# Optimization experiments

Hardware: AMD Instinct MI355X
Metric: run time of the kernel (lower is better)

Reference implementation:

```python
import jax, jax.numpy as jnp
import numpy as np

B, C, H, W, T = 16, 1024, 32, 32, 77
NUM_HEADS = 8


def setup_inputs() -> dict:
    key = jax.random.key(0)
    ks = jax.random.split(key, 8)
    s = 0.02
    return {
        "Vx": jax.random.normal(ks[0], (B, C, H, W), dtype=jnp.float32),
        "Tx": jax.random.normal(ks[1], (B, C, T), dtype=jnp.float32),
        "Wq": jax.random.normal(ks[2], (C, C), dtype=jnp.float32) * s,
        "bq": jax.random.normal(ks[3], (C,), dtype=jnp.float32) * s,
        "Wkv": jax.random.normal(ks[4], (2 * C, C), dtype=jnp.float32) * s,
        "bkv": jax.random.normal(ks[5], (2 * C,), dtype=jnp.float32) * s,
        "Wp": jax.random.normal(ks[6], (C, C), dtype=jnp.float32) * s,
        "bp": jax.random.normal(ks[7], (C,), dtype=jnp.float32) * s,
    }


def reference(Vx, Tx, Wq, bq, Wkv, bkv, Wp, bp):
    b, c, h, w = Vx.shape
    n = h * w
    nh = NUM_HEADS
    hd = c // nh
    scale = float(hd) ** (-0.5)  # scale = (dim/num_heads)**-0.5

    # 1x1 conv2d q projection: (B,C,H,W) -> (B,nh,hd,N)
    q = jnp.einsum("bchw,dc->bdhw", Vx, Wq) + bq[None, :, None, None]
    q = q.reshape(b, nh, hd, n)

    # 1x1 conv1d kv projection: (B,C,T) -> (B,nh,2*hd,T), then per-head split
    kv = jnp.einsum("bct,dc->bdt", Tx, Wkv) + bkv[None, :, None]
    kv = kv.reshape(b, nh, 2 * hd, -1)
    k, v = kv[:, :, :hd, :], kv[:, :, hd:, :]

    # attn: (B,nh,N,T) = q^T k, softmax over T
    attn = jax.nn.softmax(jnp.einsum("bhdn,bhdt->bhnt", q, k) * scale, axis=-1)

    # out: v @ attn^T -> (B,nh,hd,N) -> (B,C,H,W)
    out = jnp.einsum("bhdt,bhnt->bhdn", v, attn).reshape(b, c, h, w)

    # 1x1 conv2d output projection
    return jnp.einsum("bchw,dc->bdhw", out, Wp) + bp[None, :, None, None]
```

## Files before the change

kernel.cpp:

```cpp
#include <hip/hip_runtime.h>
#include <cstdint>
#include <cstddef>

typedef unsigned short u16;
typedef __bf16 bf16x8 __attribute__((ext_vector_type(8)));
typedef float f32x4 __attribute__((ext_vector_type(4)));

typedef __attribute__((address_space(1))) const void global_cvoid;
typedef __attribute__((address_space(3))) void lds_void;

__device__ __forceinline__ void async16(void* lds, const void* g) {
  __builtin_amdgcn_global_load_lds((global_cvoid*)g, (lds_void*)lds, 16, 0, 0);
}

__device__ __forceinline__ u16 f2bf(float f) {
  uint32_t u = __float_as_uint(f);
  return (u16)((u + 0x7fffu + ((u >> 16) & 1u)) >> 16);
}

__device__ __forceinline__ void pack4_hlh(uint32_t* dst, const float* v) {
  u16 h[4], l[4];
#pragma unroll
  for (int u = 0; u < 4; ++u) {
    h[u] = f2bf(v[u]);
    float hf = __uint_as_float((uint32_t)h[u] << 16);
    l[u] = f2bf(v[u] - hf);
  }
  dst[0] = (uint32_t)h[0] | ((uint32_t)l[0] << 16);
  dst[1] = (uint32_t)h[0] | ((uint32_t)h[1] << 16);
  dst[2] = (uint32_t)l[1] | ((uint32_t)h[1] << 16);
  dst[3] = (uint32_t)h[2] | ((uint32_t)l[2] << 16);
  dst[4] = (uint32_t)h[2] | ((uint32_t)h[3] << 16);
  dst[5] = (uint32_t)l[3] | ((uint32_t)h[3] << 16);
}

__device__ __forceinline__ void pack4_hhl(uint32_t* dst, const float* v) {
  u16 h[4], l[4];
#pragma unroll
  for (int u = 0; u < 4; ++u) {
    h[u] = f2bf(v[u]);
    float hf = __uint_as_float((uint32_t)h[u] << 16);
    l[u] = f2bf(v[u] - hf);
  }
  dst[0] = (uint32_t)h[0] | ((uint32_t)h[0] << 16);
  dst[1] = (uint32_t)l[0] | ((uint32_t)h[1] << 16);
  dst[2] = (uint32_t)h[1] | ((uint32_t)l[1] << 16);
  dst[3] = (uint32_t)h[2] | ((uint32_t)h[2] << 16);
  dst[4] = (uint32_t)l[2] | ((uint32_t)h[3] << 16);
  dst[5] = (uint32_t)h[3] | ((uint32_t)l[3] << 16);
}

__global__ __launch_bounds__(256) void pack_w(const float* __restrict__ W,
                                              u16* __restrict__ out) {
  int idx = blockIdx.x * 256 + threadIdx.x;
  int d = idx >> 10, c = idx & 1023;
  float f = W[idx];
  u16 h = f2bf(f);
  float hf = __uint_as_float((uint32_t)h << 16);
  u16 l = f2bf(f - hf);
  u16* dst = out + (size_t)d * 3072 + 3 * c;
  dst[0] = h; dst[1] = h; dst[2] = l;
}

__global__ __launch_bounds__(256) void pack_x(const float* __restrict__ X,
                                              u16* __restrict__ out) {
  const int b = blockIdx.z, c0 = blockIdx.y * 32, n0 = blockIdx.x * 32;
  __shared__ float tile[32][33];
  const float* src = X + ((size_t)b * 1024 + c0) * 1024 + n0;
  const int tc = threadIdx.x >> 5, tn = threadIdx.x & 31;
#pragma unroll
  for (int i = 0; i < 4; ++i)
    tile[tc + i * 8][tn] = src[(size_t)(tc + i * 8) * 1024 + tn];
  __syncthreads();
  const int nl = threadIdx.x >> 3, cg = (threadIdx.x & 7) * 4;
  float v[4];
#pragma unroll
  for (int u = 0; u < 4; ++u) v[u] = tile[cg + u][nl];
  uint32_t* dst = (uint32_t*)(out + ((size_t)b * 1024 + n0 + nl) * 3072 +
                              (size_t)(c0 + cg) * 3);
  pack4_hlh(dst, v);
}

__global__ __launch_bounds__(256) void pack_tx(const float* __restrict__ Tx,
                                               u16* __restrict__ out) {
  const int b = blockIdx.z, c0 = blockIdx.y * 32, t0 = blockIdx.x * 32;
  __shared__ float tile[32][33];
  const float* src = Tx + ((size_t)b * 1024 + c0) * 77;
  const int tc = threadIdx.x >> 5, tn = threadIdx.x & 31;
#pragma unroll
  for (int i = 0; i < 4; ++i) {
    int t = t0 + tn;
    tile[tc + i * 8][tn] = (t < 77) ? src[(size_t)(tc + i * 8) * 77 + t] : 0.f;
  }
  __syncthreads();
  const int nl = threadIdx.x >> 3, cg = (threadIdx.x & 7) * 4;
  float v[4];
#pragma unroll
  for (int u = 0; u < 4; ++u) v[u] = tile[cg + u][nl];
  uint32_t* dst = (uint32_t*)(out + ((size_t)b * 128 + t0 + nl) * 3072 +
                              (size_t)(c0 + cg) * 3);
  pack4_hlh(dst, v);
}

__global__ __launch_bounds__(256) void pack_kt(const float* __restrict__ kv,
                                               u16* __restrict__ out) {
  const int h = blockIdx.x, b = blockIdx.y;
  __shared__ float sk[128][81];
  const float* src = kv + ((size_t)b * 2048 + h * 256) * 80;
#pragma unroll
  for (int it = 0; it < 40; ++it) {
    int idx = it * 256 + threadIdx.x;
    sk[idx / 80][idx % 80] = src[idx];
  }
  __syncthreads();
#pragma unroll
  for (int it = 0; it < 10; ++it) {
    int idx = it * 256 + threadIdx.x;
    int t = idx >> 5, dg = (idx & 31) * 4;
    float v[4];
#pragma unroll
    for (int u = 0; u < 4; ++u) v[u] = sk[dg + u][t];
    uint32_t* dst = (uint32_t*)(out + ((size_t)(b * 8 + h) * 80 + t) * 384 +
                                (size_t)3 * dg);
    pack4_hhl(dst, v);
  }
}

__global__ __launch_bounds__(256) void pack_v(const float* __restrict__ kv,
                                              u16* __restrict__ out) {
  const int h = blockIdx.x, b = blockIdx.y;
  const float* src = kv + ((size_t)b * 2048 + h * 256 + 128) * 80;
  u16* ob = out + (size_t)(b * 8 + h) * 128 * 256;
#pragma unroll
  for (int it = 0; it < 10; ++it) {
    int idx = it * 256 + threadIdx.x;
    int d = idx / 20, tg = idx % 20;
    float4 v4 = *(const float4*)(src + (size_t)d * 80 + tg * 4);
    float v[4] = {v4.x, v4.y, v4.z, v4.w};
    uint32_t* dst = (uint32_t*)(ob + (size_t)d * 256 + 12 * tg);
    pack4_hlh(dst, v);
  }
  {
    int row = threadIdx.x >> 1, part = threadIdx.x & 1;
    *(uint4*)(ob + (size_t)row * 256 + 240 + part * 8) = make_uint4(0, 0, 0, 0);
  }
}

template <int OUTMODE>
__global__ __launch_bounds__(512, 2) void gemm_mfma(
    const u16* __restrict__ Apk, const u16* __restrict__ Bpk,
    const float* __restrict__ bias, void* __restrict__ Yv)
{
  const int b  = blockIdx.z;
  const int d0 = blockIdx.y * 256;
  const int n0 = blockIdx.x * 256;
  const int tid  = threadIdx.x;
  const int lane = tid & 63;
  const int w    = tid >> 6;
  const int wm   = w >> 2, wn = w & 3;
  const int lr   = lane & 15;
  const int lkb  = (lane >> 4) * 16;

  __shared__ __align__(16) char smem[131072];

  const u16* Bb = Bpk + (size_t)b * 1024 * 3072;

  const char* gsrc[4];
  int ldst[4];
#pragma unroll
  for (int f = 0; f < 4; ++f) {
    int g = w * 4 + f;
    if (g < 16) {
      gsrc[f] = (const char*)(Apk + (size_t)(d0 + g * 16 + lr) * 3072) + lkb;
      ldst[f] = g * 1024;
    } else {
      gsrc[f] = (const char*)(Bb + (size_t)(n0 + (g - 16) * 16 + lr) * 3072) + lkb;
      ldst[f] = 16384 + (g - 16) * 1024;
    }
  }

  auto stage = [&](int t) {
    char* base = smem + (t & 3) * 32768;
#pragma unroll
    for (int f = 0; f < 4; ++f)
      async16(base + ldst[f], gsrc[f] + (size_t)t * 64);
  };

  f32x4 acc[8][4];
#pragma unroll
  for (int i = 0; i < 8; ++i)
#pragma unroll
    for (int j = 0; j < 4; ++j) acc[i][j] = (f32x4){0.f, 0.f, 0.f, 0.f};

  stage(0); stage(1); stage(2); stage(3);
  asm volatile("s_waitcnt vmcnt(12)" ::: "memory");
  __builtin_amdgcn_s_barrier();

  for (int t = 0; t < 96; ++t) {
    const char* bufA = smem + (size_t)(t & 3) * 32768 + (size_t)lane * 16;
    const char* bufB = bufA + 16384;

    bf16x8 af[4], bfv[4];
#pragma unroll
    for (int i = 0; i < 4; ++i)
      af[i] = *(const bf16x8*)(bufA + (wm * 8 + i) * 1024);
#pragma unroll
    for (int j = 0; j < 4; ++j)
      bfv[j] = *(const bf16x8*)(bufB + (wn * 4 + j) * 1024);
    asm volatile("" ::: "memory");
    __builtin_amdgcn_s_barrier();
    asm volatile("s_waitcnt lgkmcnt(0)" ::: "memory");
    __builtin_amdgcn_sched_barrier(0);
    __builtin_amdgcn_s_setprio(1);
#pragma unroll
    for (int i = 0; i < 4; ++i)
#pragma unroll
      for (int j = 0; j < 4; ++j)
        acc[i][j] = __builtin_amdgcn_mfma_f32_16x16x32_bf16(af[i], bfv[j], acc[i][j], 0, 0, 0);
    __builtin_amdgcn_s_setprio(0);

#pragma unroll
    for (int i = 0; i < 4; ++i)
      af[i] = *(const bf16x8*)(bufA + (wm * 8 + 4 + i) * 1024);
    asm volatile("s_waitcnt lgkmcnt(0)" ::: "memory");
    __builtin_amdgcn_sched_barrier(0);
    if (t < 93)       asm volatile("s_waitcnt vmcnt(8)" ::: "memory");
    else if (t == 93) asm volatile("s_waitcnt vmcnt(4)" ::: "memory");
    else if (t == 94) asm volatile("s_waitcnt vmcnt(0)" ::: "memory");
    __builtin_amdgcn_s_barrier();
    if (t + 4 < 96) stage(t + 4);
    __builtin_amdgcn_s_setprio(1);
#pragma unroll
    for (int i = 0; i < 4; ++i)
#pragma unroll
      for (int j = 0; j < 4; ++j)
        acc[4 + i][j] = __builtin_amdgcn_mfma_f32_16x16x32_bf16(af[i], bfv[j], acc[4 + i][j], 0, 0, 0);
    __builtin_amdgcn_s_setprio(0);
  }

#pragma unroll
  for (int i = 0; i < 8; ++i) {
    const int dbase = d0 + wm * 128 + i * 16 + (lane >> 4) * 4;
    const float4 bv = *(const float4*)(bias + dbase);
#pragma unroll
    for (int j = 0; j < 4; ++j) {
      const int n = n0 + wn * 64 + j * 16 + lr;
      if (OUTMODE == 0) {
        float* yp = (float*)Yv + ((size_t)b * 1024 + dbase) * 1024 + n;
        yp[0]        = acc[i][j].x + bv.x;
        yp[1024]     = acc[i][j].y + bv.y;
        yp[2 * 1024] = acc[i][j].z + bv.z;
        yp[3 * 1024] = acc[i][j].w + bv.w;
      } else {
        float v[4] = {acc[i][j].x + bv.x, acc[i][j].y + bv.y,
                      acc[i][j].z + bv.z, acc[i][j].w + bv.w};
        uint32_t* dst = (uint32_t*)((u16*)Yv +
                                    ((size_t)b * 1024 + n) * 3072 + 3 * dbase);
        pack4_hlh(dst, v);
      }
    }
  }
}

__global__ __launch_bounds__(256) void gemm_kv_mfma(
    const u16* __restrict__ Apk, const u16* __restrict__ Bpk,
    const float* __restrict__ bias, float* __restrict__ Y)
{
  const int b  = blockIdx.y;
  const int d0 = blockIdx.x * 128;
  const int tid  = threadIdx.x;
  const int lane = tid & 63;
  const int w    = tid >> 6;
  const int wm   = w >> 1, wn = w & 1;

  __shared__ __align__(16) char smem[65536];

  const int lr = lane & 15;
  const int lk = (lane >> 4) * 8;

  const u16* Bb = Bpk + (size_t)b * 128 * 3072;
  const char* gA0 = (const char*)(Apk + ((size_t)(d0 + (w * 2 + 0) * 16 + lr) * 3072 + lk));
  const char* gA1 = (const char*)(Apk + ((size_t)(d0 + (w * 2 + 1) * 16 + lr) * 3072 + lk));
  const char* gB0 = (const char*)(Bb  + ((size_t)((w * 2 + 0) * 16 + lr) * 3072 + lk));
  const char* gB1 = (const char*)(Bb  + ((size_t)((w * 2 + 1) * 16 + lr) * 3072 + lk));

  auto stage = [&](int p, int ks) {
    char* ba = smem + p * 32768 + (w * 2) * 1024;
    char* bb = ba + 16384;
    const int kb = ks * 128;
#pragma unroll
    for (int k2 = 0; k2 < 2; ++k2) {
      async16(ba + k2 * 8192,        gA0 + kb + k2 * 64);
      async16(ba + k2 * 8192 + 1024, gA1 + kb + k2 * 64);
      async16(bb + k2 * 8192,        gB0 + kb + k2 * 64);
      async16(bb + k2 * 8192 + 1024, gB1 + kb + k2 * 64);
    }
  };

  f32x4 acc[4][4];
#pragma unroll
  for (int i = 0; i < 4; ++i)
#pragma unroll
    for (int j = 0; j < 4; ++j) acc[i][j] = (f32x4){0.f, 0.f, 0.f, 0.f};

  stage(0, 0);
  stage(1, 1);

  for (int ks = 0; ks < 48; ++ks) {
    if (ks < 47) asm volatile("s_waitcnt vmcnt(8)" ::: "memory");
    else         asm volatile("s_waitcnt vmcnt(0)" ::: "memory");
    __builtin_amdgcn_s_barrier();

    const int p = ks & 1;
    const char* baseA = smem + p * 32768 + wm * 4096 + lane * 16;
    const char* baseB = smem + p * 32768 + 16384 + wn * 4096 + lane * 16;
#pragma unroll
    for (int k2 = 0; k2 < 2; ++k2) {
      bf16x8 af[4], bfv[4];
#pragma unroll
      for (int i = 0; i < 4; ++i) {
        af[i]  = *(const bf16x8*)(baseA + k2 * 8192 + i * 1024);
        bfv[i] = *(const bf16x8*)(baseB + k2 * 8192 + i * 1024);
      }
#pragma unroll
      for (int i = 0; i < 4; ++i)
#pragma unroll
        for (int j = 0; j < 4; ++j)
          acc[i][j] = __builtin_amdgcn_mfma_f32_16x16x32_bf16(af[i], bfv[j], acc[i][j], 0, 0, 0);
    }

    asm volatile("" ::: "memory");
    __builtin_amdgcn_s_barrier();
    if (ks + 2 < 48) stage(p, ks + 2);
  }

#pragma unroll
  for (int i = 0; i < 4; ++i) {
    const int dbase = d0 + wm * 64 + i * 16 + (lane >> 4) * 4;
    const float4 bv = *(const float4*)(bias + dbase);
#pragma unroll
    for (int j = 0; j < 4; ++j) {
      const int n = wn * 64 + j * 16 + lr;
      if (n < 80) {
        float* yp = Y + ((size_t)b * 2048 + dbase) * 80 + n;
        yp[0]      = acc[i][j].x + bv.x;
        yp[80]     = acc[i][j].y + bv.y;
        yp[160]    = acc[i][j].z + bv.z;
        yp[240]    = acc[i][j].w + bv.w;
      }
    }
  }
}

__global__ __launch_bounds__(256, 2) void attn_mfma(
    const u16* __restrict__ qpk,
    const u16* __restrict__ ktpk,
    const u16* __restrict__ vpk,
    u16* __restrict__ xout)
{
  const int b  = blockIdx.z;
  const int h  = blockIdx.y;
  const int n0 = blockIdx.x * 128;
  const int tid  = threadIdx.x;
  const int w    = tid >> 6;
  const int lane = tid & 63;
  const int lr = lane & 15;
  const int lc = lane >> 4;
  const float scale = 0.08838834764831845f;

  __shared__ u16 Plds[4][32 * 256];
  u16* Pw = &Plds[w][0];

  {
    int row = lane & 31, part = lane >> 5;
    *(uint4*)&Pw[row * 256 + 240 + part * 8] = make_uint4(0, 0, 0, 0);
  }

  const u16* qb = qpk + ((size_t)b * 1024 + n0 + w * 32 + lr) * 3072 +
                  384 * h + lc * 8;
  const u16* kb = ktpk + (size_t)(b * 8 + h) * 80 * 384 + (size_t)lr * 384 + lc * 8;

  f32x4 accs[2][5];
#pragma unroll
  for (int ni = 0; ni < 2; ++ni)
#pragma unroll
    for (int tt = 0; tt < 5; ++tt) accs[ni][tt] = (f32x4){0.f, 0.f, 0.f, 0.f};

  for (int ks = 0; ks < 12; ++ks) {
    bf16x8 qa[2], kt[5];
    qa[0] = *(const bf16x8*)(qb + ks * 32);
    qa[1] = *(const bf16x8*)(qb + 16 * 3072 + ks * 32);
#pragma unroll
    for (int tt = 0; tt < 5; ++tt)
      kt[tt] = *(const bf16x8*)(kb + (size_t)tt * 16 * 384 + ks * 32);
#pragma unroll
    for (int ni = 0; ni < 2; ++ni)
#pragma unroll
      for (int tt = 0; tt < 5; ++tt)
        accs[ni][tt] = __builtin_amdgcn_mfma_f32_16x16x32_bf16(qa[ni], kt[tt], accs[ni][tt], 0, 0, 0);
  }

  if (lr >= 13) {
    accs[0][4] = (f32x4){-3.0e38f, -3.0e38f, -3.0e38f, -3.0e38f};
    accs[1][4] = (f32x4){-3.0e38f, -3.0e38f, -3.0e38f, -3.0e38f};
  }

#pragma unroll
  for (int ni = 0; ni < 2; ++ni) {
    f32x4 mx = accs[ni][0];
#pragma unroll
    for (int tt = 1; tt < 5; ++tt) {
      mx.x = fmaxf(mx.x, accs[ni][tt].x);
      mx.y = fmaxf(mx.y, accs[ni][tt].y);
      mx.z = fmaxf(mx.z, accs[ni][tt].z);
      mx.w = fmaxf(mx.w, accs[ni][tt].w);
    }
#pragma unroll
    for (int mk = 1; mk <= 8; mk <<= 1) {
      mx.x = fmaxf(mx.x, __shfl_xor(mx.x, mk));
      mx.y = fmaxf(mx.y, __shfl_xor(mx.y, mk));
      mx.z = fmaxf(mx.z, __shfl_xor(mx.z, mk));
      mx.w = fmaxf(mx.w, __shfl_xor(mx.w, mk));
    }
    f32x4 sm = (f32x4){0.f, 0.f, 0.f, 0.f};
#pragma unroll
    for (int tt = 0; tt < 5; ++tt) {
      f32x4 e;
      e.x = __expf((accs[ni][tt].x - mx.x) * scale);
      e.y = __expf((accs[ni][tt].y - mx.y) * scale);
      e.z = __expf((accs[ni][tt].z - mx.z) * scale);
      e.w = __expf((accs[ni][tt].w - mx.w) * scale);
      accs[ni][tt] = e;
      sm += e;
    }
#pragma unroll
    for (int mk = 1; mk <= 8; mk <<= 1) {
      sm.x += __shfl_xor(sm.x, mk);
      sm.y += __shfl_xor(sm.y, mk);
      sm.z += __shfl_xor(sm.z, mk);
      sm.w += __shfl_xor(sm.w, mk);
    }
    f32x4 inv = (f32x4){1.f / sm.x, 1.f / sm.y, 1.f / sm.z, 1.f / sm.w};
#pragma unroll
    for (int tt = 0; tt < 5; ++tt) {
#pragma unroll
      for (int c = 0; c < 4; ++c) {
        float pv = accs[ni][tt][c] * inv[c];
        int row = ni * 16 + lc * 4 + c;
        int t = tt * 16 + lr;
        u16 hh = f2bf(pv);
        float hf = __uint_as_float((uint32_t)hh << 16);
        u16 ll = f2bf(pv - hf);
        u16* pp = &Pw[row * 256 + 3 * t];
        pp[0] = hh; pp[1] = hh; pp[2] = ll;
      }
    }
  }

  f32x4 acco[2][8];
#pragma unroll
  for (int ni = 0; ni < 2; ++ni)
#pragma unroll
    for (int dj = 0; dj < 8; ++dj) acco[ni][dj] = (f32x4){0.f, 0.f, 0.f, 0.f};

  const u16* vb = vpk + (size_t)(b * 8 + h) * 128 * 256 + (size_t)lr * 256 + lc * 8;
  const u16* pb = &Pw[lr * 256 + lc * 8];

  for (int ks = 0; ks < 8; ++ks) {
    bf16x8 pa[2], vv[8];
    pa[0] = *(const bf16x8*)(pb + ks * 32);
    pa[1] = *(const bf16x8*)(pb + 16 * 256 + ks * 32);
#pragma unroll
    for (int dj = 0; dj < 8; ++dj)
      vv[dj] = *(const bf16x8*)(vb + (size_t)dj * 16 * 256 + ks * 32);
#pragma unroll
    for (int ni = 0; ni < 2; ++ni)
#pragma unroll
      for (int dj = 0; dj < 8; ++dj)
        acco[ni][dj] = __builtin_amdgcn_mfma_f32_16x16x32_bf16(pa[ni], vv[dj], acco[ni][dj], 0, 0, 0);
  }

  float* Pf = (float*)Pw;
#pragma unroll
  for (int ni = 0; ni < 2; ++ni)
#pragma unroll
    for (int dj = 0; dj < 8; ++dj) {
      const int dl = dj * 16 + lr;
#pragma unroll
      for (int c = 0; c < 4; ++c)
        Pf[(ni * 16 + lc * 4 + c) * 128 + dl] = acco[ni][dj][c];
    }

  const int prow = lane >> 5;
  const int pgrp = lane & 31;
#pragma unroll
  for (int r2 = 0; r2 < 16; ++r2) {
    const int row = r2 * 2 + prow;
    f32x4 vv4 = *(const f32x4*)&Pf[row * 128 + pgrp * 4];
    float v[4] = {vv4.x, vv4.y, vv4.z, vv4.w};
    uint32_t* dst = (uint32_t*)(xout +
        ((size_t)b * 1024 + n0 + w * 32 + row) * 3072 + 384 * h + 12 * pgrp);
    pack4_hlh(dst, v);
  }
}

extern "C" void kernel_launch(void* const* d_in, const int* in_sizes, int n_in,
                              void* d_out, int out_size, void* d_ws, size_t ws_size,
                              hipStream_t stream) {
  const float* Vx  = (const float*)d_in[0];
  const float* Tx  = (const float*)d_in[1];
  const float* Wq  = (const float*)d_in[2];
  const float* bq  = (const float*)d_in[3];
  const float* Wkv = (const float*)d_in[4];
  const float* bkv = (const float*)d_in[5];
  const float* Wp  = (const float*)d_in[6];
  const float* bp  = (const float*)d_in[7];
  float* out = (float*)d_out;

  char* ws = (char*)d_ws;
  const size_t MiB = (size_t)1 << 20;
  u16*   Xpk      = (u16*)(ws + 0);
  u16*   qpk      = (u16*)(ws + 96 * MiB);
  u16*   WqPk     = (u16*)(ws + 192 * MiB);
  u16*   KTpk     = (u16*)(ws + 192 * MiB);
  u16*   WkvPk    = (u16*)(ws + 198 * MiB);
  u16*   Vpk      = (u16*)(ws + 200 * MiB);
  u16*   TxPk     = (u16*)(ws + 210 * MiB);
  float* kvbuf    = (float*)(ws + 222 * MiB);
  u16*   WpPk     = (u16*)(ws + 233 * MiB);

  pack_w<<<4096, 256, 0, stream>>>(Wq, WqPk);
  pack_w<<<4096, 256, 0, stream>>>(Wp, WpPk);
  pack_w<<<8192, 256, 0, stream>>>(Wkv, WkvPk);
  pack_x<<<dim3(32, 32, 16), 256, 0, stream>>>(Vx, Xpk);
  pack_tx<<<dim3(4, 32, 16), 256, 0, stream>>>(Tx, TxPk);
  gemm_mfma<1><<<dim3(4, 4, 16), 512, 0, stream>>>(WqPk, Xpk, bq, qpk);
  gemm_kv_mfma<<<dim3(16, 16), 256, 0, stream>>>(WkvPk, TxPk, bkv, kvbuf);
  pack_kt<<<dim3(8, 16), 256, 0, stream>>>(kvbuf, KTpk);
  pack_v<<<dim3(8, 16), 256, 0, stream>>>(kvbuf, Vpk);
  attn_mfma<<<dim3(8, 8, 16), 256, 0, stream>>>(qpk, KTpk, Vpk, Xpk);
  gemm_mfma<0><<<dim3(4, 4, 16), 512, 0, stream>>>(WpPk, Xpk, bp, out);
}
```

Measured before the change: 544.0 us.

## Deepen kv GEMM pipeline to four stages and drop mid-iteration barrier in main GEMM

```diff
diff --git a/kernel.cpp b/kernel.cpp
--- a/kernel.cpp
+++ b/kernel.cpp
@@ -200,17 +200,13 @@
     const char* bufA = smem + (size_t)(t & 3) * 32768 + (size_t)lane * 16;
     const char* bufB = bufA + 16384;
 
-    bf16x8 af[4], bfv[4];
+    bf16x8 af[4], bfv[4], af2[4];
 #pragma unroll
     for (int i = 0; i < 4; ++i)
       af[i] = *(const bf16x8*)(bufA + (wm * 8 + i) * 1024);
 #pragma unroll
     for (int j = 0; j < 4; ++j)
       bfv[j] = *(const bf16x8*)(bufB + (wn * 4 + j) * 1024);
-    asm volatile("" ::: "memory");
-    __builtin_amdgcn_s_barrier();
-    asm volatile("s_waitcnt lgkmcnt(0)" ::: "memory");
-    __builtin_amdgcn_sched_barrier(0);
     __builtin_amdgcn_s_setprio(1);
 #pragma unroll
     for (int i = 0; i < 4; ++i)
@@ -221,20 +217,21 @@
 
 #pragma unroll
     for (int i = 0; i < 4; ++i)
-      af[i] = *(const bf16x8*)(bufA + (wm * 8 + 4 + i) * 1024);
+      af2[i] = *(const bf16x8*)(bufA + (wm * 8 + 4 + i) * 1024);
     asm volatile("s_waitcnt lgkmcnt(0)" ::: "memory");
     __builtin_amdgcn_sched_barrier(0);
     if (t < 93)       asm volatile("s_waitcnt vmcnt(8)" ::: "memory");
     else if (t == 93) asm volatile("s_waitcnt vmcnt(4)" ::: "memory");
-    else if (t == 94) asm volatile("s_waitcnt vmcnt(0)" ::: "memory");
+    else              asm volatile("s_waitcnt vmcnt(0)" ::: "memory");
     __builtin_amdgcn_s_barrier();
+    asm volatile("" ::: "memory");
     if (t + 4 < 96) stage(t + 4);
     __builtin_amdgcn_s_setprio(1);
 #pragma unroll
     for (int i = 0; i < 4; ++i)
 #pragma unroll
       for (int j = 0; j < 4; ++j)
-        acc[4 + i][j] = __builtin_amdgcn_mfma_f32_16x16x32_bf16(af[i], bfv[j], acc[4 + i][j], 0, 0, 0);
+        acc[4 + i][j] = __builtin_amdgcn_mfma_f32_16x16x32_bf16(af2[i], bfv[j], acc[4 + i][j], 0, 0, 0);
     __builtin_amdgcn_s_setprio(0);
   }
 
@@ -272,29 +269,30 @@
   const int lane = tid & 63;
   const int w    = tid >> 6;
   const int wm   = w >> 1, wn = w & 1;
+  const int lr   = lane & 15;
+  const int lkb  = (lane >> 4) * 16;
 
   __shared__ __align__(16) char smem[65536];
 
-  const int lr = lane & 15;
-  const int lk = (lane >> 4) * 8;
-
   const u16* Bb = Bpk + (size_t)b * 128 * 3072;
-  const char* gA0 = (const char*)(Apk + ((size_t)(d0 + (w * 2 + 0) * 16 + lr) * 3072 + lk));
-  const char* gA1 = (const char*)(Apk + ((size_t)(d0 + (w * 2 + 1) * 16 + lr) * 3072 + lk));
-  const char* gB0 = (const char*)(Bb  + ((size_t)((w * 2 + 0) * 16 + lr) * 3072 + lk));
-  const char* gB1 = (const char*)(Bb  + ((size_t)((w * 2 + 1) * 16 + lr) * 3072 + lk));
-
-  auto stage = [&](int p, int ks) {
-    char* ba = smem + p * 32768 + (w * 2) * 1024;
-    char* bb = ba + 16384;
-    const int kb = ks * 128;
-#pragma unroll
-    for (int k2 = 0; k2 < 2; ++k2) {
-      async16(ba + k2 * 8192,        gA0 + kb + k2 * 64);
-      async16(ba + k2 * 8192 + 1024, gA1 + kb + k2 * 64);
-      async16(bb + k2 * 8192,        gB0 + kb + k2 * 64);
-      async16(bb + k2 * 8192 + 1024, gB1 + kb + k2 * 64);
-    }
+
+  const char* gsrc[4];
+  int ldst[4];
+#pragma unroll
+  for (int f = 0; f < 4; ++f) {
+    int g = w * 4 + f;
+    if (g < 8)
+      gsrc[f] = (const char*)(Apk + (size_t)(d0 + g * 16 + lr) * 3072) + lkb;
+    else
+      gsrc[f] = (const char*)(Bb + (size_t)((g - 8) * 16 + lr) * 3072) + lkb;
+    ldst[f] = g * 1024;
+  }
+
+  auto stage = [&](int t) {
+    char* base = smem + (t & 3) * 16384;
+#pragma unroll
+    for (int f = 0; f < 4; ++f)
+      async16(base + ldst[f], gsrc[f] + (size_t)t * 64);
   };
 
   f32x4 acc[4][4];
@@ -303,35 +301,45 @@
 #pragma unroll
     for (int j = 0; j < 4; ++j) acc[i][j] = (f32x4){0.f, 0.f, 0.f, 0.f};
 
-  stage(0, 0);
-  stage(1, 1);
-
-  for (int ks = 0; ks < 48; ++ks) {
-    if (ks < 47) asm volatile("s_waitcnt vmcnt(8)" ::: "memory");
-    else         asm volatile("s_waitcnt vmcnt(0)" ::: "memory");
+  stage(0); stage(1); stage(2); stage(3);
+  asm volatile("s_waitcnt vmcnt(12)" ::: "memory");
+  __builtin_amdgcn_s_barrier();
+
+  for (int t = 0; t < 96; ++t) {
+    const char* bufA = smem + (size_t)(t & 3) * 16384 + (size_t)lane * 16;
+    const char* bufB = bufA + 8192;
+
+    bf16x8 af[4], bfv[4];
+#pragma unroll
+    for (int j = 0; j < 4; ++j)
+      bfv[j] = *(const bf16x8*)(bufB + (wn * 4 + j) * 1024);
+    af[0] = *(const bf16x8*)(bufA + (wm * 4 + 0) * 1024);
+    af[1] = *(const bf16x8*)(bufA + (wm * 4 + 1) * 1024);
+    __builtin_amdgcn_s_setprio(1);
+#pragma unroll
+    for (int i = 0; i < 2; ++i)
+#pragma unroll
+      for (int j = 0; j < 4; ++j)
+        acc[i][j] = __builtin_amdgcn_mfma_f32_16x16x32_bf16(af[i], bfv[j], acc[i][j], 0, 0, 0);
+    __builtin_amdgcn_s_setprio(0);
+
+    af[2] = *(const bf16x8*)(bufA + (wm * 4 + 2) * 1024);
+    af[3] = *(const bf16x8*)(bufA + (wm * 4 + 3) * 1024);
+    asm volatile("s_waitcnt lgkmcnt(0)" ::: "memory");
+    __builtin_amdgcn_sched_barrier(0);
+    if (t < 93)       asm volatile("s_waitcnt vmcnt(8)" ::: "memory");
+    else if (t == 93) asm volatile("s_waitcnt vmcnt(4)" ::: "memory");
+    else              asm volatile("s_waitcnt vmcnt(0)" ::: "memory");
     __builtin_amdgcn_s_barrier();
-
-    const int p = ks & 1;
-    const char* baseA = smem + p * 32768 + wm * 4096 + lane * 16;
-    const char* baseB = smem + p * 32768 + 16384 + wn * 4096 + lane * 16;
-#pragma unroll
-    for (int k2 = 0; k2 < 2; ++k2) {
-      bf16x8 af[4], bfv[4];
-#pragma unroll
-      for (int i = 0; i < 4; ++i) {
-        af[i]  = *(const bf16x8*)(baseA + k2 * 8192 + i * 1024);
-        bfv[i] = *(const bf16x8*)(baseB + k2 * 8192 + i * 1024);
-      }
-#pragma unroll
-      for (int i = 0; i < 4; ++i)
-#pragma unroll
-        for (int j = 0; j < 4; ++j)
-          acc[i][j] = __builtin_amdgcn_mfma_f32_16x16x32_bf16(af[i], bfv[j], acc[i][j], 0, 0, 0);
-    }
-
     asm volatile("" ::: "memory");
-    __builtin_amdgcn_s_barrier();
-    if (ks + 2 < 48) stage(p, ks + 2);
+    if (t + 4 < 96) stage(t + 4);
+    __builtin_amdgcn_s_setprio(1);
+#pragma unroll
+    for (int i = 2; i < 4; ++i)
+#pragma unroll
+      for (int j = 0; j < 4; ++j)
+        acc[i][j] = __builtin_amdgcn_mfma_f32_16x16x32_bf16(af[i], bfv[j], acc[i][j], 0, 0, 0);
+    __builtin_amdgcn_s_setprio(0);
   }
 
 #pragma unroll
@@ -386,6 +394,7 @@
 #pragma unroll
     for (int tt = 0; tt < 5; ++tt) accs[ni][tt] = (f32x4){0.f, 0.f, 0.f, 0.f};
 
+#pragma unroll 2
   for (int ks = 0; ks < 12; ++ks) {
     bf16x8 qa[2], kt[5];
     qa[0] = *(const bf16x8*)(qb + ks * 32);
```

Measured after the change: 530.6 us. -2.4%, faster.
